# Optimization experiments

Measured on AMD Instinct MI355X. Metric: run time of the kernel, lower is better.

The kernel has to match this reference:

```python
import jax, jax.numpy as jnp
import numpy as np

WS = 7   # window size
SS = 3   # shift size


def _ln(x, g, b):
    m = x.mean(-1, keepdims=True)
    v = ((x - m) ** 2).mean(-1, keepdims=True)
    return (x - m) / jnp.sqrt(v + 1e-5) * g + b


def setup_inputs() -> dict:
    key = jax.random.key(0)
    ks = jax.random.split(key, 8)
    B, H, W, C, nh = 64, 56, 56, 96, 3
    N = WS * WS
    x = jax.random.normal(ks[0], (B, H * W, C), jnp.float32)

    # Swin SW-MSA attention mask: [nW, N, N], 0 where attention is allowed, -100 otherwise
    img = np.zeros((H, W), np.int32)
    cnt = 0
    for hs in (slice(0, H - WS), slice(H - WS, H - SS), slice(H - SS, None)):
        for wsl in (slice(0, W - WS), slice(W - WS, W - SS), slice(W - SS, None)):
            img[hs, wsl] = cnt
            cnt += 1
    win = img.reshape(H // WS, WS, W // WS, WS).transpose(0, 2, 1, 3).reshape(-1, N)
    am = np.where(win[:, None, :] != win[:, :, None], -100.0, 0.0).astype(np.float32)

    # relative position index: [N, N] in [0, (2*WS-1)^2)
    coords = np.stack(np.meshgrid(np.arange(WS), np.arange(WS), indexing='ij')).reshape(2, -1)
    rel = (coords[:, :, None] - coords[:, None, :]).transpose(1, 2, 0)
    rel[..., 0] += WS - 1
    rel[..., 1] += WS - 1
    rel[..., 0] *= 2 * WS - 1
    rel_index = jnp.asarray(rel.sum(-1), jnp.int32)

    p = lambda k, sh: jax.random.normal(k, sh, jnp.float32) * 0.02
    return dict(
        x=x,
        attn_mask=jnp.asarray(am),
        rel_index=rel_index,
        norm1_g=jnp.ones((C,), jnp.float32), norm1_b=jnp.zeros((C,), jnp.float32),
        qkv_w=p(ks[1], (3 * C, C)), qkv_b=jnp.zeros((3 * C,), jnp.float32),
        rel_bias_table=p(ks[2], ((2 * WS - 1) ** 2, nh)),
        proj_w=p(ks[3], (C, C)), proj_b=jnp.zeros((C,), jnp.float32),
        norm2_g=jnp.ones((C,), jnp.float32), norm2_b=jnp.zeros((C,), jnp.float32),
        fc1_w=p(ks[4], (4 * C, C)), fc1_b=jnp.zeros((4 * C,), jnp.float32),
        fc2_w=p(ks[5], (C, 4 * C)), fc2_b=jnp.zeros((C,), jnp.float32),
        H=56, W=56,
    )


def reference(x, attn_mask, rel_index, norm1_g, norm1_b, qkv_w, qkv_b,
              rel_bias_table, proj_w, proj_b, norm2_g, norm2_b,
              fc1_w, fc1_b, fc2_w, fc2_b, H, W):
    B, L, C = x.shape
    nh = rel_bias_table.shape[1]
    d = C // nh
    N = WS * WS
    shortcut = x

    xn = _ln(x, norm1_g, norm1_b).reshape(B, H, W, C)
    # cyclic shift (H%WS==0, W%WS==0 so no padding needed)
    xs = jnp.roll(xn, (-SS, -SS), axis=(1, 2))
    # window partition -> [B*nW, N, C]
    xw = xs.reshape(B, H // WS, WS, W // WS, WS, C).transpose(0, 1, 3, 2, 4, 5).reshape(-1, N, C)
    B_ = xw.shape[0]
    nW = attn_mask.shape[0]

    qkv = (xw @ qkv_w.T + qkv_b).reshape(B_, N, 3, nh, d).transpose(2, 0, 3, 1, 4)
    q, k, v = qkv[0] * (d ** -0.5), qkv[1], qkv[2]  # [B_, nh, N, d]
    attn = jnp.einsum('bhnd,bhmd->bhnm', q, k)
    bias = rel_bias_table[rel_index.reshape(-1)].reshape(N, N, nh).transpose(2, 0, 1)
    attn = attn + bias[None]
    attn = attn.reshape(B_ // nW, nW, nh, N, N) + attn_mask[None, :, None]
    attn = jax.nn.softmax(attn.reshape(B_, nh, N, N), axis=-1)
    out = jnp.einsum('bhnm,bhmd->bhnd', attn, v).transpose(0, 2, 1, 3).reshape(B_, N, C)
    out = out @ proj_w.T + proj_b

    # window reverse + reverse cyclic shift
    xr = out.reshape(B, H // WS, W // WS, WS, WS, C).transpose(0, 1, 3, 2, 4, 5).reshape(B, H, W, C)
    xr = jnp.roll(xr, (SS, SS), axis=(1, 2)).reshape(B, L, C)

    x = shortcut + xr
    h = _ln(x, norm2_g, norm2_b)
    h = jax.nn.gelu(h @ fc1_w.T + fc1_b, approximate=False) @ fc2_w.T + fc2_b
    return x + h
```

## Files before the change

### kernel.cpp

```cpp
#include <hip/hip_runtime.h>
#include <hip/hip_bf16.h>

typedef __attribute__((ext_vector_type(8))) short short8;
typedef __attribute__((ext_vector_type(4))) float f32x4;

constexpr int HW = 56;

constexpr int SR    = 104;
constexpr int SVT   = 200;
constexpr int OFF_X = 0;
constexpr int OFF_Q = 64 * SR;
constexpr int OFF_K = 2 * 64 * SR;
constexpr int OFF_V = 3 * 64 * SR;
constexpr int POOLN = OFF_V + 32 * SVT;
constexpr int BUF0  = 0;
constexpr int BUF1  = 9216;
constexpr int YN    = OFF_V;
constexpr int YSTR  = 96;

constexpr int WQKV  = 0;
constexpr int WPROJ = 27648;
constexpr int WFC1  = 36864;
constexpr int WFC2  = 73728;
constexpr int WTOT  = 110592;
constexpr int BIASN = 64 * 3 * 49 * 64;
constexpr size_t WS_M1 = (size_t)WTOT * 2;
constexpr size_t WS_M2 = WS_M1 + (size_t)BIASN * 4;

__device__ __forceinline__ ushort bfc(float f) {
  union { __hip_bfloat16 h; ushort u; } v;
  v.h = __float2bfloat16(f);
  return v.u;
}
__device__ __forceinline__ uint pk2(float a, float b) {
  union { __hip_bfloat162 h2; uint u; } v;
  v.h2 = __float22bfloat162_rn(make_float2(a, b));
  return v.u;
}
__device__ __forceinline__ void st4(short* p, float a, float b, float c, float d) {
  uint2 u; u.x = pk2(a, b); u.y = pk2(c, d);
  *(uint2*)p = u;
}
__device__ __forceinline__ short8 ldw8(const float* p) {
  float4 a = *(const float4*)p;
  float4 b = *(const float4*)(p + 4);
  short8 r;
  r[0] = (short)bfc(a.x); r[1] = (short)bfc(a.y); r[2] = (short)bfc(a.z); r[3] = (short)bfc(a.w);
  r[4] = (short)bfc(b.x); r[5] = (short)bfc(b.y); r[6] = (short)bfc(b.z); r[7] = (short)bfc(b.w);
  return r;
}
template<bool PRE>
__device__ __forceinline__ short8 wfrag(const short* wsb, int ts, int lane, const float* fsrc) {
  if constexpr (PRE) return *(const short8*)&wsb[(ts << 9) + lane * 8];
  else               return ldw8(fsrc);
}
__device__ __forceinline__ float gelu(float v) {
  return v * __builtin_amdgcn_rcpf(1.0f + __expf(-1.702f * v));
}
__device__ __forceinline__ short8 repack(f32x4 A, f32x4 B, int ln, int gq) {
  uint a_lo = pk2(A[0], A[1]), a_hi = pk2(A[2], A[3]);
  uint b_lo = pk2(B[0], B[1]), b_hi = pk2(B[2], B[3]);
  int s0 = ln + (((2 * gq)     & 3) << 4);
  int s1 = ln + (((2 * gq + 1) & 3) << 4);
  uint A0 = __shfl(a_lo, s0, 64), B0 = __shfl(b_lo, s0, 64);
  uint A1 = __shfl(a_hi, s0, 64), B1 = __shfl(b_hi, s0, 64);
  uint A2 = __shfl(a_lo, s1, 64), B2 = __shfl(b_lo, s1, 64);
  uint A3 = __shfl(a_hi, s1, 64), B3 = __shfl(b_hi, s1, 64);
  bool uA = (gq < 2);
  union { uint u[4]; short8 s8; } r;
  r.u[0] = uA ? A0 : B0; r.u[1] = uA ? A1 : B1;
  r.u[2] = uA ? A2 : B2; r.u[3] = uA ? A3 : B3;
  return r.s8;
}
__device__ __forceinline__ void stage18(const short* g0, short* l0, int wv, int lane) {
  #pragma unroll
  for (int i = 0; i < 5; ++i) {
    int s = wv + 4 * i;
    if (s < 18)
      __builtin_amdgcn_global_load_lds((const unsigned int*)(g0 + (s << 9) + lane * 8),
                                       (unsigned int*)(l0 + (s << 9)), 16, 0, 0);
  }
}

__global__ __launch_bounds__(256) void cvt_weights(
    const float* __restrict__ qkv_w, const float* __restrict__ proj_w,
    const float* __restrict__ fc1_w, const float* __restrict__ fc2_w,
    short* __restrict__ ws)
{
  int idx = blockIdx.x * 256 + threadIdx.x;
  if (idx >= WTOT) return;
  int j = idx & 7, lane = (idx >> 3) & 63;
  int cl = lane & 15;
  int g  = 8 * (lane >> 4) + j;
  float v;
  if (idx < WPROJ) {
    int ts = idx >> 9; int tile = ts / 3, s = ts - 3 * tile;
    v = qkv_w[(size_t)(16 * tile + cl) * 96 + 32 * s + g];
    if (tile < 6) v *= 0.17677669529663687f;
  } else if (idx < WFC1) {
    int ts = (idx - WPROJ) >> 9; int tile = ts / 3, s = ts - 3 * tile;
    v = proj_w[(size_t)(16 * tile + cl) * 96 + 32 * s + g];
  } else if (idx < WFC2) {
    int ts = (idx - WFC1) >> 9; int T = ts / 3, s = ts - 3 * T;
    int cn = T / 6, nt = T - 6 * cn;
    v = fc1_w[(size_t)(96 * cn + 16 * nt + cl) * 96 + 32 * s + g];
  } else {
    int ts = (idx - WFC2) >> 9; int T = ts / 3, s = ts - 3 * T;
    int cn = T / 6, nt = T - 6 * cn;
    v = fc2_w[(size_t)(16 * nt + cl) * 384 + 96 * cn + 32 * s + g];
  }
  ws[idx] = (short)bfc(v);
}

__global__ __launch_bounds__(256) void prep_bias(
    const float* __restrict__ attn_mask, const int* __restrict__ rel_index,
    const float* __restrict__ rel_tab, float* __restrict__ bias3)
{
  int idx = blockIdx.x * 256 + threadIdx.x;
  if (idx >= BIASN) return;
  int k = idx & 63;
  int t = idx >> 6;
  int q = t % 49;
  int wh = t / 49;
  int h = wh % 3, w = wh / 3;
  float v = -1e30f;
  if (k < 49) {
    int qk = q * 49 + k;
    v = rel_tab[rel_index[qk] * 3 + h] + attn_mask[(size_t)w * 2401 + qk];
  }
  bias3[idx] = v;
}

template<int MODE>
__global__ __launch_bounds__(256, 3) void swin_mfma_kernel(
    const float* __restrict__ x,
    const float* __restrict__ attn_mask,
    const int*   __restrict__ rel_index,
    const float* __restrict__ n1g, const float* __restrict__ n1b,
    const float* __restrict__ qkv_w, const float* __restrict__ qkv_b,
    const float* __restrict__ rel_tab,
    const float* __restrict__ proj_w, const float* __restrict__ proj_b,
    const float* __restrict__ n2g, const float* __restrict__ n2b,
    const float* __restrict__ fc1_w, const float* __restrict__ fc1_b,
    const float* __restrict__ fc2_w, const float* __restrict__ fc2_b,
    const short* __restrict__ wsw,
    const float* __restrict__ bias3,
    float* __restrict__ out)
{
  constexpr bool PRE = (MODE >= 1);
  __shared__ alignas(16) short pool[POOLN];
  short* buf0 = pool + BUF0;
  short* buf1 = pool + BUF1;

  const int tid  = threadIdx.x;
  const int wv   = tid >> 6;
  const int lane = tid & 63;
  const int ln   = lane & 15;
  const int gq   = lane >> 4;
  const int bw   = blockIdx.x;
  const int b    = bw >> 6, widx = bw & 63;
  const int wr   = widx >> 3, wc = widx & 7;

  const f32x4 zf = {0.f, 0.f, 0.f, 0.f};
  const int qq = 16 * wv + ln;

  auto gbase = [&](int n) -> size_t {
    int i = n / 7, j = n - 7 * i;
    int h = wr * 7 + i + 3; if (h >= HW) h -= HW;
    int w = wc * 7 + j + 3; if (w >= HW) w -= HW;
    return ((size_t)b * (HW * HW) + (size_t)h * HW + w) * 96;
  };
  const size_t obase = gbase(qq < 49 ? qq : 48);

  float xraw[6][4];
  {
    if (qq < 49) {
      const float* xr = x + obase;
      #pragma unroll
      for (int nt = 0; nt < 6; ++nt) {
        float4 v = *(const float4*)&xr[16 * nt + 4 * gq];
        xraw[nt][0] = v.x; xraw[nt][1] = v.y; xraw[nt][2] = v.z; xraw[nt][3] = v.w;
      }
    } else {
      #pragma unroll
      for (int nt = 0; nt < 6; ++nt)
        xraw[nt][0] = xraw[nt][1] = xraw[nt][2] = xraw[nt][3] = 0.f;
    }
    float s1 = 0.f, s2 = 0.f;
    #pragma unroll
    for (int nt = 0; nt < 6; ++nt)
      #pragma unroll
      for (int r = 0; r < 4; ++r) { s1 += xraw[nt][r]; s2 += xraw[nt][r] * xraw[nt][r]; }
    s1 += __shfl_xor(s1, 16, 64); s1 += __shfl_xor(s1, 32, 64);
    s2 += __shfl_xor(s2, 16, 64); s2 += __shfl_xor(s2, 32, 64);
    float mean = s1 * (1.f / 96.f);
    float inv  = rsqrtf(s2 * (1.f / 96.f) - mean * mean + 1e-5f);
    #pragma unroll
    for (int nt = 0; nt < 6; ++nt) {
      float4 g4 = *(const float4*)&n1g[16 * nt + 4 * gq];
      float4 b4 = *(const float4*)&n1b[16 * nt + 4 * gq];
      st4(&pool[OFF_X + qq * SR + 16 * nt + 4 * gq],
          (xraw[nt][0] - mean) * inv * g4.x + b4.x,
          (xraw[nt][1] - mean) * inv * g4.y + b4.y,
          (xraw[nt][2] - mean) * inv * g4.z + b4.z,
          (xraw[nt][3] - mean) * inv * g4.w + b4.w);
    }
  }
  __syncthreads();

  {
    short8 af[3][4];
    #pragma unroll
    for (int s = 0; s < 3; ++s)
      #pragma unroll
      for (int m = 0; m < 4; ++m)
        af[s][m] = *(const short8*)&pool[OFF_X + (16 * m + ln) * SR + 32 * s + 8 * gq];

    const float sc_ = 0.17677669529663687f;
    for (int t = wv; t < 18; t += 4) {
      short8 wf[3];
      #pragma unroll
      for (int s = 0; s < 3; ++s)
        wf[s] = wfrag<PRE>(wsw + WQKV, t * 3 + s, lane,
                           qkv_w + (size_t)(16 * t + ln) * 96 + 32 * s + 8 * gq);
      int which = t / 6;
      if (which == 2) {
        int d  = 16 * (t - 12) + ln;
        float bv = qkv_b[192 + d];
        int dd = d & 31, hh = d >> 5;
        __builtin_amdgcn_s_setprio(1);
        #pragma unroll
        for (int m = 0; m < 4; ++m) {
          f32x4 acc = zf;
          #pragma unroll
          for (int s = 0; s < 3; ++s)
            acc = __builtin_amdgcn_mfma_f32_16x16x32_bf16(af[s][m], wf[s], acc, 0, 0, 0);
          st4(&pool[OFF_V + dd * SVT + hh * 64 + 16 * m + 4 * gq],
              acc[0] + bv, acc[1] + bv, acc[2] + bv, acc[3] + bv);
        }
        __builtin_amdgcn_s_setprio(0);
      } else {
        float4 b4 = *(const float4*)&qkv_b[16 * t + 4 * gq];
        if (which == 0) {
          if constexpr (PRE) { b4.x *= sc_; b4.y *= sc_; b4.z *= sc_; b4.w *= sc_; }
        }
        __builtin_amdgcn_s_setprio(1);
        #pragma unroll
        for (int m = 0; m < 4; ++m) {
          f32x4 acc = zf;
          #pragma unroll
          for (int s = 0; s < 3; ++s)
            acc = __builtin_amdgcn_mfma_f32_16x16x32_bf16(wf[s], af[s][m], acc, 0, 0, 0);
          int tok = 16 * m + ln;
          float v0 = acc[0] + b4.x, v1 = acc[1] + b4.y, v2 = acc[2] + b4.z, v3 = acc[3] + b4.w;
          if (which == 0) {
            if constexpr (PRE)
              st4(&pool[OFF_Q + tok * SR + 16 * t + 4 * gq], v0, v1, v2, v3);
            else
              st4(&pool[OFF_Q + tok * SR + 16 * t + 4 * gq], v0 * sc_, v1 * sc_, v2 * sc_, v3 * sc_);
          } else {
            st4(&pool[OFF_K + tok * SR + 16 * (t - 6) + 4 * gq], v0, v1, v2, v3);
          }
        }
        __builtin_amdgcn_s_setprio(0);
      }
    }
  }
  __syncthreads();

  const int qc = qq < 49 ? qq : 48;
  int   relvv[4][4];
  float maskb[4][4];
  if constexpr (MODE < 2) {
    #pragma unroll
    for (int nt = 0; nt < 4; ++nt)
      #pragma unroll
      for (int r = 0; r < 4; ++r) {
        int key = 16 * nt + 4 * gq + r;
        if (key < 49) {
          int qk = qc * 49 + key;
          relvv[nt][r] = rel_index[qk];
          maskb[nt][r] = attn_mask[(size_t)widx * 2401 + qk];
        } else {
          relvv[nt][r] = 0;
          maskb[nt][r] = -1e30f;
        }
      }
  }
  const float* bph = nullptr;
  if constexpr (MODE == 2) bph = bias3 + ((size_t)widx * 3 * 49 + qc) * 64;

  for (int h = 0; h < 3; ++h) {
    short8 bq = *(const short8*)&pool[OFF_Q + qq * SR + h * 32 + 8 * gq];
    f32x4 sc[4];
    __builtin_amdgcn_s_setprio(1);
    #pragma unroll
    for (int nt = 0; nt < 4; ++nt) {
      f32x4 bia;
      if constexpr (MODE == 2) {
        bia = *(const f32x4*)&bph[h * 3136 + 16 * nt + 4 * gq];
      } else {
        #pragma unroll
        for (int r = 0; r < 4; ++r)
          bia[r] = rel_tab[relvv[nt][r] * 3 + h] + maskb[nt][r];
      }
      short8 ak = *(const short8*)&pool[OFF_K + (16 * nt + ln) * SR + h * 32 + 8 * gq];
      sc[nt] = __builtin_amdgcn_mfma_f32_16x16x32_bf16(ak, bq, bia, 0, 0, 0);
    }
    __builtin_amdgcn_s_setprio(0);
    f32x4 pv[4];
    float sum = 0.f;
    #pragma unroll
    for (int nt = 0; nt < 4; ++nt)
      #pragma unroll
      for (int r = 0; r < 4; ++r) { pv[nt][r] = __expf(sc[nt][r]); sum += pv[nt][r]; }
    sum += __shfl_xor(sum, 16, 64);
    sum += __shfl_xor(sum, 32, 64);
    float inv = __builtin_amdgcn_rcpf(sum);
    #pragma unroll
    for (int nt = 0; nt < 4; ++nt)
      #pragma unroll
      for (int r = 0; r < 4; ++r) pv[nt][r] *= inv;
    short8 bp0 = repack(pv[0], pv[1], ln, gq);
    short8 bp1 = repack(pv[2], pv[3], ln, gq);
    __builtin_amdgcn_s_setprio(1);
    #pragma unroll
    for (int dt = 0; dt < 2; ++dt) {
      short8 av0 = *(const short8*)&pool[OFF_V + (16 * dt + ln) * SVT + h * 64 + 8 * gq];
      short8 av1 = *(const short8*)&pool[OFF_V + (16 * dt + ln) * SVT + h * 64 + 32 + 8 * gq];
      f32x4 o = __builtin_amdgcn_mfma_f32_16x16x32_bf16(av0, bp0, zf, 0, 0, 0);
      o = __builtin_amdgcn_mfma_f32_16x16x32_bf16(av1, bp1, o, 0, 0, 0);
      st4(&pool[OFF_Q + qq * SR + h * 32 + 16 * dt + 4 * gq], o[0], o[1], o[2], o[3]);
    }
    __builtin_amdgcn_s_setprio(0);
  }

  short8 ao[3];
  #pragma unroll
  for (int s = 0; s < 3; ++s)
    ao[s] = *(const short8*)&pool[OFF_Q + qq * SR + 32 * s + 8 * gq];
  __syncthreads();

  if constexpr (PRE) stage18(wsw + WPROJ, buf0, wv, lane);
  __syncthreads();

  if constexpr (PRE) stage18(wsw + WFC1, buf1, wv, lane);
  float y[6][4];
  __builtin_amdgcn_s_setprio(1);
  #pragma unroll
  for (int nt = 0; nt < 6; ++nt) {
    f32x4 acc = zf;
    #pragma unroll
    for (int s = 0; s < 3; ++s) {
      short8 wfr = PRE ? *(const short8*)&buf0[((nt * 3 + s) << 9) + lane * 8]
                       : ldw8(proj_w + (size_t)(16 * nt + ln) * 96 + 32 * s + 8 * gq);
      acc = __builtin_amdgcn_mfma_f32_16x16x32_bf16(wfr, ao[s], acc, 0, 0, 0);
    }
    float4 pb = *(const float4*)&proj_b[16 * nt + 4 * gq];
    y[nt][0] = acc[0] + pb.x + xraw[nt][0];
    y[nt][1] = acc[1] + pb.y + xraw[nt][1];
    y[nt][2] = acc[2] + pb.z + xraw[nt][2];
    y[nt][3] = acc[3] + pb.w + xraw[nt][3];
  }
  __builtin_amdgcn_s_setprio(0);
  {
    float s1 = 0.f, s2 = 0.f;
    #pragma unroll
    for (int nt = 0; nt < 6; ++nt)
      #pragma unroll
      for (int r = 0; r < 4; ++r) { s1 += y[nt][r]; s2 += y[nt][r] * y[nt][r]; }
    s1 += __shfl_xor(s1, 16, 64); s1 += __shfl_xor(s1, 32, 64);
    s2 += __shfl_xor(s2, 16, 64); s2 += __shfl_xor(s2, 32, 64);
    float mean = s1 * (1.f / 96.f);
    float inv  = rsqrtf(s2 * (1.f / 96.f) - mean * mean + 1e-5f);
    #pragma unroll
    for (int nt = 0; nt < 6; ++nt) {
      float4 g4 = *(const float4*)&n2g[16 * nt + 4 * gq];
      float4 b4 = *(const float4*)&n2b[16 * nt + 4 * gq];
      st4(&pool[YN + qq * YSTR + 16 * nt + 4 * gq],
          (y[nt][0] - mean) * inv * g4.x + b4.x,
          (y[nt][1] - mean) * inv * g4.y + b4.y,
          (y[nt][2] - mean) * inv * g4.z + b4.z,
          (y[nt][3] - mean) * inv * g4.w + b4.w);
    }
  }
  short8 ay[3];
  #pragma unroll
  for (int s = 0; s < 3; ++s)
    ay[s] = *(const short8*)&pool[YN + qq * YSTR + 32 * s + 8 * gq];
  __syncthreads();

  f32x4 accO[6] = {zf, zf, zf, zf, zf, zf};
  short8 hq[3];
  #pragma unroll
  for (int cn = 0; cn < 4; ++cn) {
    if constexpr (PRE) stage18(wsw + WFC2 + (cn * 18) * 512, buf0, wv, lane);
    f32x4 ha[6];
    __builtin_amdgcn_s_setprio(1);
    #pragma unroll
    for (int nt = 0; nt < 6; ++nt) {
      f32x4 acc = zf;
      #pragma unroll
      for (int s = 0; s < 3; ++s) {
        short8 wfr = PRE ? *(const short8*)&buf1[((nt * 3 + s) << 9) + lane * 8]
                         : ldw8(fc1_w + (size_t)(96 * cn + 16 * nt + ln) * 96 + 32 * s + 8 * gq);
        acc = __builtin_amdgcn_mfma_f32_16x16x32_bf16(wfr, ay[s], acc, 0, 0, 0);
      }
      float4 b1 = *(const float4*)&fc1_b[96 * cn + 16 * nt + 4 * gq];
      ha[nt][0] = gelu(acc[0] + b1.x);
      ha[nt][1] = gelu(acc[1] + b1.y);
      ha[nt][2] = gelu(acc[2] + b1.z);
      ha[nt][3] = gelu(acc[3] + b1.w);
    }
    __builtin_amdgcn_s_setprio(0);
    #pragma unroll
    for (int s = 0; s < 3; ++s) hq[s] = repack(ha[2 * s], ha[2 * s + 1], ln, gq);
    __syncthreads();

    if constexpr (PRE) { if (cn < 3) stage18(wsw + WFC1 + ((cn + 1) * 18) * 512, buf1, wv, lane); }
    __builtin_amdgcn_s_setprio(1);
    #pragma unroll
    for (int nt = 0; nt < 6; ++nt) {
      #pragma unroll
      for (int s = 0; s < 3; ++s) {
        short8 wfr = PRE ? *(const short8*)&buf0[((nt * 3 + s) << 9) + lane * 8]
                         : ldw8(fc2_w + (size_t)(16 * nt + ln) * 384 + 96 * cn + 32 * s + 8 * gq);
        accO[nt] = __builtin_amdgcn_mfma_f32_16x16x32_bf16(wfr, hq[s], accO[nt], 0, 0, 0);
      }
    }
    __builtin_amdgcn_s_setprio(0);
    if (cn < 3) __syncthreads();
  }

  if (qq < 49) {
    float* dst = out + obase;
    #pragma unroll
    for (int nt = 0; nt < 6; ++nt) {
      float4 fb = *(const float4*)&fc2_b[16 * nt + 4 * gq];
      float4 v;
      v.x = y[nt][0] + accO[nt][0] + fb.x;
      v.y = y[nt][1] + accO[nt][1] + fb.y;
      v.z = y[nt][2] + accO[nt][2] + fb.z;
      v.w = y[nt][3] + accO[nt][3] + fb.w;
      *(float4*)&dst[16 * nt + 4 * gq] = v;
    }
  }
}

extern "C" void kernel_launch(void* const* d_in, const int* in_sizes, int n_in,
                              void* d_out, int out_size, void* d_ws, size_t ws_size,
                              hipStream_t stream) {
  const float* x         = (const float*)d_in[0];
  const float* attn_mask = (const float*)d_in[1];
  const int*   rel_index = (const int*)  d_in[2];
  const float* n1g       = (const float*)d_in[3];
  const float* n1b       = (const float*)d_in[4];
  const float* qkv_w     = (const float*)d_in[5];
  const float* qkv_b     = (const float*)d_in[6];
  const float* rel_tab   = (const float*)d_in[7];
  const float* proj_w    = (const float*)d_in[8];
  const float* proj_b    = (const float*)d_in[9];
  const float* n2g       = (const float*)d_in[10];
  const float* n2b       = (const float*)d_in[11];
  const float* fc1_w     = (const float*)d_in[12];
  const float* fc1_b     = (const float*)d_in[13];
  const float* fc2_w     = (const float*)d_in[14];
  const float* fc2_b     = (const float*)d_in[15];
  float* out = (float*)d_out;

  const int B = in_sizes[0] / (HW * HW * 96);
  const bool m1 = ws_size >= WS_M1;
  const bool m2 = ws_size >= WS_M2;
  short* ws    = (short*)d_ws;
  float* bias3 = (float*)((char*)d_ws + WS_M1);

  if (m1)
    cvt_weights<<<(WTOT + 255) / 256, 256, 0, stream>>>(qkv_w, proj_w, fc1_w, fc2_w, ws);
  if (m2)
    prep_bias<<<(BIASN + 255) / 256, 256, 0, stream>>>(attn_mask, rel_index, rel_tab, bias3);

  if (m2)
    swin_mfma_kernel<2><<<B * 64, 256, 0, stream>>>(
        x, attn_mask, rel_index, n1g, n1b, qkv_w, qkv_b, rel_tab, proj_w, proj_b,
        n2g, n2b, fc1_w, fc1_b, fc2_w, fc2_b, (const short*)ws, (const float*)bias3, out);
  else if (m1)
    swin_mfma_kernel<1><<<B * 64, 256, 0, stream>>>(
        x, attn_mask, rel_index, n1g, n1b, qkv_w, qkv_b, rel_tab, proj_w, proj_b,
        n2g, n2b, fc1_w, fc1_b, fc2_w, fc2_b, (const short*)ws, (const float*)nullptr, out);
  else
    swin_mfma_kernel<0><<<B * 64, 256, 0, stream>>>(
        x, attn_mask, rel_index, n1g, n1b, qkv_w, qkv_b, rel_tab, proj_w, proj_b,
        n2g, n2b, fc1_w, fc1_b, fc2_w, fc2_b, (const short*)nullptr, (const float*)nullptr, out);
}
```

Baseline: 161.2 us.

## Replace shuffle-based repack with LDS round-trip and remap weight staging buffers

Removes the cross-lane shuffle repack of softmax probabilities and GELU activations. Each result is now stored as bf16 into the row-per-query LDS region and read back in MFMA operand layout. Weight staging buffers are relocated (buf0 into the K region, buf1 split across the X/Q region and a tail) so the activation scratch can reuse the Q rows. The fc loop is also no longer fully unrolled. The aim is to cut shuffle instruction count and register pressure, at the cost of extra LDS traffic and possible aliasing or bank-conflict hazards.

```diff
diff --git a/kernel.cpp b/kernel.cpp
--- a/kernel.cpp
+++ b/kernel.cpp
@@ -13,10 +13,6 @@
 constexpr int OFF_K = 2 * 64 * SR;
 constexpr int OFF_V = 3 * 64 * SR;
 constexpr int POOLN = OFF_V + 32 * SVT;
-constexpr int BUF0  = 0;
-constexpr int BUF1  = 9216;
-constexpr int YN    = OFF_V;
-constexpr int YSTR  = 96;
 
 constexpr int WQKV  = 0;
 constexpr int WPROJ = 27648;
@@ -57,28 +53,22 @@
 __device__ __forceinline__ float gelu(float v) {
   return v * __builtin_amdgcn_rcpf(1.0f + __expf(-1.702f * v));
 }
-__device__ __forceinline__ short8 repack(f32x4 A, f32x4 B, int ln, int gq) {
-  uint a_lo = pk2(A[0], A[1]), a_hi = pk2(A[2], A[3]);
-  uint b_lo = pk2(B[0], B[1]), b_hi = pk2(B[2], B[3]);
-  int s0 = ln + (((2 * gq)     & 3) << 4);
-  int s1 = ln + (((2 * gq + 1) & 3) << 4);
-  uint A0 = __shfl(a_lo, s0, 64), B0 = __shfl(b_lo, s0, 64);
-  uint A1 = __shfl(a_hi, s0, 64), B1 = __shfl(b_hi, s0, 64);
-  uint A2 = __shfl(a_lo, s1, 64), B2 = __shfl(b_lo, s1, 64);
-  uint A3 = __shfl(a_hi, s1, 64), B3 = __shfl(b_hi, s1, 64);
-  bool uA = (gq < 2);
-  union { uint u[4]; short8 s8; } r;
-  r.u[0] = uA ? A0 : B0; r.u[1] = uA ? A1 : B1;
-  r.u[2] = uA ? A2 : B2; r.u[3] = uA ? A3 : B3;
-  return r.s8;
-}
-__device__ __forceinline__ void stage18(const short* g0, short* l0, int wv, int lane) {
+__device__ __forceinline__ short* b0set(short* pool, int s) {
+  return pool + OFF_K + (s << 9);
+}
+__device__ __forceinline__ short* b1set(short* pool, int s) {
+  return pool + (s < 13 ? (s << 9) : 22528 + ((s - 13) << 9));
+}
+template<bool B1>
+__device__ __forceinline__ void stage18(const short* g0, short* pool, int wv, int lane) {
   #pragma unroll
   for (int i = 0; i < 5; ++i) {
     int s = wv + 4 * i;
-    if (s < 18)
+    if (s < 18) {
+      short* dst = B1 ? b1set(pool, s) : b0set(pool, s);
       __builtin_amdgcn_global_load_lds((const unsigned int*)(g0 + (s << 9) + lane * 8),
-                                       (unsigned int*)(l0 + (s << 9)), 16, 0, 0);
+                                       (unsigned int*)dst, 16, 0, 0);
+    }
   }
 }
 
@@ -149,8 +139,6 @@
 {
   constexpr bool PRE = (MODE >= 1);
   __shared__ alignas(16) short pool[POOLN];
-  short* buf0 = pool + BUF0;
-  short* buf1 = pool + BUF1;
 
   const int tid  = threadIdx.x;
   const int wv   = tid >> 6;
@@ -308,7 +296,7 @@
       sc[nt] = __builtin_amdgcn_mfma_f32_16x16x32_bf16(ak, bq, bia, 0, 0, 0);
     }
     __builtin_amdgcn_s_setprio(0);
-    f32x4 pv[4];
+    float pv[4][4];
     float sum = 0.f;
     #pragma unroll
     for (int nt = 0; nt < 4; ++nt)
@@ -319,10 +307,11 @@
     float inv = __builtin_amdgcn_rcpf(sum);
     #pragma unroll
     for (int nt = 0; nt < 4; ++nt)
-      #pragma unroll
-      for (int r = 0; r < 4; ++r) pv[nt][r] *= inv;
-    short8 bp0 = repack(pv[0], pv[1], ln, gq);
-    short8 bp1 = repack(pv[2], pv[3], ln, gq);
+      st4(&pool[OFF_X + qq * SR + 16 * nt + 4 * gq],
+          pv[nt][0] * inv, pv[nt][1] * inv, pv[nt][2] * inv, pv[nt][3] * inv);
+
+    short8 bp0 = *(const short8*)&pool[OFF_X + qq * SR + 8 * gq];
+    short8 bp1 = *(const short8*)&pool[OFF_X + qq * SR + 32 + 8 * gq];
     __builtin_amdgcn_s_setprio(1);
     #pragma unroll
     for (int dt = 0; dt < 2; ++dt) {
@@ -341,10 +330,10 @@
     ao[s] = *(const short8*)&pool[OFF_Q + qq * SR + 32 * s + 8 * gq];
   __syncthreads();
 
-  if constexpr (PRE) stage18(wsw + WPROJ, buf0, wv, lane);
+  if constexpr (PRE) stage18<false>(wsw + WPROJ, pool, wv, lane);
   __syncthreads();
 
-  if constexpr (PRE) stage18(wsw + WFC1, buf1, wv, lane);
+  if constexpr (PRE) stage18<true>(wsw + WFC1, pool, wv, lane);
   float y[6][4];
   __builtin_amdgcn_s_setprio(1);
   #pragma unroll
@@ -352,7 +341,7 @@
     f32x4 acc = zf;
     #pragma unroll
     for (int s = 0; s < 3; ++s) {
-      short8 wfr = PRE ? *(const short8*)&buf0[((nt * 3 + s) << 9) + lane * 8]
+      short8 wfr = PRE ? *(const short8*)(b0set(pool, nt * 3 + s) + lane * 8)
                        : ldw8(proj_w + (size_t)(16 * nt + ln) * 96 + 32 * s + 8 * gq);
       acc = __builtin_amdgcn_mfma_f32_16x16x32_bf16(wfr, ao[s], acc, 0, 0, 0);
     }
@@ -377,7 +366,7 @@
     for (int nt = 0; nt < 6; ++nt) {
       float4 g4 = *(const float4*)&n2g[16 * nt + 4 * gq];
       float4 b4 = *(const float4*)&n2b[16 * nt + 4 * gq];
-      st4(&pool[YN + qq * YSTR + 16 * nt + 4 * gq],
+      st4(&pool[OFF_Q + qq * SR + 16 * nt + 4 * gq],
           (y[nt][0] - mean) * inv * g4.x + b4.x,
           (y[nt][1] - mean) * inv * g4.y + b4.y,
           (y[nt][2] - mean) * inv * g4.z + b4.z,
@@ -387,45 +376,43 @@
   short8 ay[3];
   #pragma unroll
   for (int s = 0; s < 3; ++s)
-    ay[s] = *(const short8*)&pool[YN + qq * YSTR + 32 * s + 8 * gq];
+    ay[s] = *(const short8*)&pool[OFF_Q + qq * SR + 32 * s + 8 * gq];
   __syncthreads();
 
   f32x4 accO[6] = {zf, zf, zf, zf, zf, zf};
-  short8 hq[3];
-  #pragma unroll
   for (int cn = 0; cn < 4; ++cn) {
-    if constexpr (PRE) stage18(wsw + WFC2 + (cn * 18) * 512, buf0, wv, lane);
-    f32x4 ha[6];
+    if constexpr (PRE) stage18<false>(wsw + WFC2 + (cn * 18) * 512, pool, wv, lane);
     __builtin_amdgcn_s_setprio(1);
     #pragma unroll
     for (int nt = 0; nt < 6; ++nt) {
       f32x4 acc = zf;
       #pragma unroll
       for (int s = 0; s < 3; ++s) {
-        short8 wfr = PRE ? *(const short8*)&buf1[((nt * 3 + s) << 9) + lane * 8]
+        short8 wfr = PRE ? *(const short8*)(b1set(pool, nt * 3 + s) + lane * 8)
                          : ldw8(fc1_w + (size_t)(96 * cn + 16 * nt + ln) * 96 + 32 * s + 8 * gq);
         acc = __builtin_amdgcn_mfma_f32_16x16x32_bf16(wfr, ay[s], acc, 0, 0, 0);
       }
       float4 b1 = *(const float4*)&fc1_b[96 * cn + 16 * nt + 4 * gq];
-      ha[nt][0] = gelu(acc[0] + b1.x);
-      ha[nt][1] = gelu(acc[1] + b1.y);
-      ha[nt][2] = gelu(acc[2] + b1.z);
-      ha[nt][3] = gelu(acc[3] + b1.w);
+      st4(&pool[OFF_Q + qq * SR + 16 * nt + 4 * gq],
+          gelu(acc[0] + b1.x), gelu(acc[1] + b1.y),
+          gelu(acc[2] + b1.z), gelu(acc[3] + b1.w));
     }
     __builtin_amdgcn_s_setprio(0);
-    #pragma unroll
-    for (int s = 0; s < 3; ++s) hq[s] = repack(ha[2 * s], ha[2 * s + 1], ln, gq);
+    short8 ah[3];
+    #pragma unroll
+    for (int s = 0; s < 3; ++s)
+      ah[s] = *(const short8*)&pool[OFF_Q + qq * SR + 32 * s + 8 * gq];
     __syncthreads();
 
-    if constexpr (PRE) { if (cn < 3) stage18(wsw + WFC1 + ((cn + 1) * 18) * 512, buf1, wv, lane); }
+    if constexpr (PRE) { if (cn < 3) stage18<true>(wsw + WFC1 + ((cn + 1) * 18) * 512, pool, wv, lane); }
     __builtin_amdgcn_s_setprio(1);
     #pragma unroll
     for (int nt = 0; nt < 6; ++nt) {
       #pragma unroll
       for (int s = 0; s < 3; ++s) {
-        short8 wfr = PRE ? *(const short8*)&buf0[((nt * 3 + s) << 9) + lane * 8]
+        short8 wfr = PRE ? *(const short8*)(b0set(pool, nt * 3 + s) + lane * 8)
                          : ldw8(fc2_w + (size_t)(16 * nt + ln) * 384 + 96 * cn + 32 * s + 8 * gq);
-        accO[nt] = __builtin_amdgcn_mfma_f32_16x16x32_bf16(wfr, hq[s], accO[nt], 0, 0, 0);
+        accO[nt] = __builtin_amdgcn_mfma_f32_16x16x32_bf16(wfr, ah[s], accO[nt], 0, 0, 0);
       }
     }
     __builtin_amdgcn_s_setprio(0);
```

Measured after the change: 152.1 us (median of 2 runs). 5.6% less time.
